# Optimization experiments

Hardware: AMD Instinct MI355X
Metric: run time of the kernel (lower is better)

## Reference

```python
import jax, jax.numpy as jnp
import numpy as np

SCALAR_DIM = 452          # 2 + 6 + (110+1)*4
GRID_C, GRID_H, GRID_W = 2, 32, 18
GRID_FLAT = GRID_C * GRID_H * GRID_W  # 1152
OBS_DIM = SCALAR_DIM + GRID_FLAT      # 1604
CNN_OUT, SC_OUT, HID, N_ACT = 128, 64, 128, 2305
CNN_FLAT = 64 * 8 * 5                 # 32x18 -> 16x9 -> 8x5
T, B = 256, 128


def setup_inputs() -> dict:
    key = jax.random.key(0)
    ks = jax.random.split(key, 24)
    p = lambda k, shape: jax.random.normal(k, shape, jnp.float32) * 0.02
    return dict(
        obs_seq=jax.random.uniform(ks[0], (T, B, OBS_DIM), jnp.float32),
        h0=jnp.zeros((1, B, HID), jnp.float32),
        c0=jnp.zeros((1, B, HID), jnp.float32),
        done_mask=jax.random.randint(ks[1], (T, B), 0, 2) > 0,
        conv1_w=p(ks[2], (32, GRID_C, 3, 3)), conv1_b=jnp.zeros((32,), jnp.float32),
        conv2_w=p(ks[3], (64, 32, 3, 3)),     conv2_b=jnp.zeros((64,), jnp.float32),
        conv3_w=p(ks[4], (64, 64, 3, 3)),     conv3_b=jnp.zeros((64,), jnp.float32),
        fc_w=p(ks[5], (CNN_OUT, CNN_FLAT)),   fc_b=jnp.zeros((CNN_OUT,), jnp.float32),
        s1_w=p(ks[6], (64, SCALAR_DIM)),      s1_b=jnp.zeros((64,), jnp.float32),
        s2_w=p(ks[7], (SC_OUT, 64)),          s2_b=jnp.zeros((SC_OUT,), jnp.float32),
        w_ih=p(ks[8], (4 * HID, CNN_OUT + SC_OUT)),
        w_hh=p(ks[9], (4 * HID, HID)),
        b_ih=jnp.zeros((4 * HID,), jnp.float32),
        b_hh=jnp.zeros((4 * HID,), jnp.float32),
        pol_w=p(ks[10], (N_ACT, HID)), pol_b=jnp.zeros((N_ACT,), jnp.float32),
        val_w=p(ks[11], (1, HID)),     val_b=jnp.zeros((1,), jnp.float32),
    )


def _conv(x, w, b, stride):
    y = jax.lax.conv_general_dilated(
        x, w, (stride, stride), ((1, 1), (1, 1)),
        dimension_numbers=("NCHW", "OIHW", "NCHW"))
    return y + b[None, :, None, None]


def reference(obs_seq, h0, c0, done_mask,
              conv1_w, conv1_b, conv2_w, conv2_b, conv3_w, conv3_b,
              fc_w, fc_b, s1_w, s1_b, s2_w, s2_b,
              w_ih, w_hh, b_ih, b_hh, pol_w, pol_b, val_w, val_b):
    Tt, Bb, _ = obs_seq.shape
    flat = obs_seq.reshape(Tt * Bb, -1)
    scalars = flat[:, :SCALAR_DIM]
    grid = flat[:, SCALAR_DIM:SCALAR_DIM + GRID_FLAT].reshape(-1, GRID_C, GRID_H, GRID_W)

    # CNN encoder
    x = jax.nn.relu(_conv(grid, conv1_w, conv1_b, 1))
    x = jax.nn.relu(_conv(x, conv2_w, conv2_b, 2))
    x = jax.nn.relu(_conv(x, conv3_w, conv3_b, 2))
    cnn = jax.nn.relu(x.reshape(x.shape[0], -1) @ fc_w.T + fc_b)

    # scalar MLP
    sc = jax.nn.relu(jax.nn.relu(scalars @ s1_w.T + s1_b) @ s2_w.T + s2_b)

    emb = jnp.concatenate([cnn, sc], axis=-1).reshape(Tt, Bb, -1)  # (T,B,192)

    # episode-reset mask applied BEFORE each step (for t>0, from done[t-1])
    keep = jnp.concatenate(
        [jnp.ones((1, Bb), jnp.float32),
         1.0 - done_mask[:-1].astype(jnp.float32)], axis=0)[..., None]  # (T,B,1)

    def step(carry, inp):
        h, c = carry
        x_t, k_t = inp
        h = h * k_t
        c = c * k_t
        g = x_t @ w_ih.T + h @ w_hh.T + b_ih + b_hh
        i, f, gg, o = jnp.split(g, 4, axis=-1)  # torch gate order i,f,g,o
        c = jax.nn.sigmoid(f) * c + jax.nn.sigmoid(i) * jnp.tanh(gg)
        h = jax.nn.sigmoid(o) * jnp.tanh(c)
        return (h, c), h

    (h_f, c_f), outs = jax.lax.scan(step, (h0[0], c0[0]), (emb, keep))

    logits = outs @ pol_w.T + pol_b   # (T,B,n_actions)
    values = outs @ val_w.T + val_b   # (T,B,1)
    return logits, values, h_f[None], c_f[None]
```

## Files before the change

kernel.cpp:

```cpp
#include <hip/hip_runtime.h>


typedef __attribute__((ext_vector_type(8))) short v8s;
typedef __attribute__((ext_vector_type(4))) float v4f;
typedef __attribute__((ext_vector_type(4))) unsigned int v4u;

#define DEV static __device__ __forceinline__

DEV unsigned int cvtpk(float lo, float hi){
  unsigned int d;
  asm("v_cvt_pk_bf16_f32 %0, %1, %2" : "=v"(d) : "v"(lo), "v"(hi));
  return d;
}
DEV unsigned short f2bf(float x){ return (unsigned short)(cvtpk(x, x) & 0xffffu); }
DEV float bf2f(unsigned short h){ return __uint_as_float(((unsigned int)h) << 16); }
DEV unsigned int pkbf(float a, float b){ return cvtpk(a, b); }
DEV v4f MFMA(v8s a, v8s b, v4f c){ return __builtin_amdgcn_mfma_f32_16x16x32_bf16(a, b, c, 0, 0, 0); }
DEV v4f vzero(){ v4f z = {0.f, 0.f, 0.f, 0.f}; return z; }
DEV float relu(float x){ return x > 0.f ? x : 0.f; }
DEV float sigm(float x){ return 1.0f / (1.0f + __expf(-x)); }
DEV float tanhfast(float x){
  x = fminf(15.0f, fmaxf(-15.0f, x));
  float e = __expf(2.0f * x);
  return (e - 1.0f) / (e + 1.0f);
}
DEV uint2 pack4(v4f a, float4 b){
  return make_uint2(cvtpk(relu(a[0]+b.x), relu(a[1]+b.y)),
                    cvtpk(relu(a[2]+b.z), relu(a[3]+b.w)));
}
union U8S { v4u u4; v8s s8; };

__global__ __launch_bounds__(256) void pack_kernel(
    const float* __restrict__ src, const float* __restrict__ src2,
    unsigned short* __restrict__ dst, int N, int K, int KS, int CI, int mode, int total){
  for (int idx = blockIdx.x * 256 + threadIdx.x; idx < total; idx += gridDim.x * 256){
    int e  = idx & 7;
    int l  = (idx >> 3) & 63;
    int fs = idx >> 9;
    int ks = fs % KS;
    int nt = fs / KS;
    int n = nt * 16 + (l & 15);
    int k = ks * 32 + (l >> 4) * 8 + e;
    float v = 0.f;
    if (n < N && k < K){
      if (mode == 0)      v = src[n * K + k];
      else if (mode == 1){ int p9 = k / CI, ci = k - p9 * CI; v = src[(n * CI + ci) * 9 + p9]; }
      else if (mode == 2){ int pos = k >> 6, ci = k & 63;     v = src[n * 2560 + ci * 40 + pos]; }
      else if (mode == 3) v = (k < 192) ? src[n * 192 + k] : src2[n * 128 + (k - 192)];
      else { int dy = k >> 3, r = k & 7, dx = r >> 1, ci = r & 1;
             if (dx < 3) v = src[(n * 2 + ci) * 9 + dy * 3 + dx]; }
    }
    dst[idx] = f2bf(v);
  }
}

__global__ __launch_bounds__(512) void bias_kernel(const float* __restrict__ bih,
    const float* __restrict__ bhh, float* __restrict__ bias512){
  int t = threadIdx.x;
  if (t < 512) bias512[t] = bih[t] + bhh[t];
}

__global__ __launch_bounds__(256) void mlp_kernel(const float* __restrict__ obs,
    const unsigned short* __restrict__ s1p, const unsigned short* __restrict__ s2p,
    const float* __restrict__ s1b, const float* __restrict__ s2b,
    unsigned short* __restrict__ emb){
  __shared__ __align__(16) unsigned short xl[32 * 488];
  __shared__ __align__(16) unsigned short h1[32 * 72];
  int tid = threadIdx.x, w = tid >> 6, l = tid & 63, i = l & 15, u = l >> 4;
  long s0 = (long)blockIdx.x * 32;
  for (int idx = tid; idx < 32 * 113; idx += 256){
    int r = idx / 113, q = idx - r * 113;
    float4 v = *(const float4*)&obs[(s0 + r) * 1604 + q * 4];
    *(uint2*)&xl[r * 488 + q * 4] = make_uint2(pkbf(v.x, v.y), pkbf(v.z, v.w));
  }
  for (int idx = tid; idx < 32 * 28; idx += 256){
    int r = idx / 28, k = 452 + (idx - r * 28);
    xl[r * 488 + k] = 0;
  }
  __syncthreads();
  v4f acc0 = vzero(), acc1 = vzero();
  const v8s* F1 = (const v8s*)s1p;
  #pragma unroll
  for (int ks = 0; ks < 15; ++ks){
    v8s bb = F1[(w * 15 + ks) * 64 + l];
    v8s aa0 = *(const v8s*)&xl[(0 * 16 + i) * 488 + ks * 32 + u * 8];
    v8s aa1 = *(const v8s*)&xl[(1 * 16 + i) * 488 + ks * 32 + u * 8];
    acc0 = MFMA(aa0, bb, acc0);
    acc1 = MFMA(aa1, bb, acc1);
  }
  float b1 = s1b[w * 16 + i];
  #pragma unroll
  for (int r = 0; r < 4; ++r){
    float v0 = relu(acc0[r] + b1);
    float v1 = relu(acc1[r] + b1);
    h1[(u * 4 + r) * 72 + w * 16 + i] = f2bf(v0);
    h1[(16 + u * 4 + r) * 72 + w * 16 + i] = f2bf(v1);
  }
  __syncthreads();
  v4f a20 = vzero(), a21 = vzero();
  const v8s* F2 = (const v8s*)s2p;
  #pragma unroll
  for (int ks = 0; ks < 2; ++ks){
    v8s bb = F2[(w * 2 + ks) * 64 + l];
    v8s aa0 = *(const v8s*)&h1[(0 * 16 + i) * 72 + ks * 32 + u * 8];
    v8s aa1 = *(const v8s*)&h1[(1 * 16 + i) * 72 + ks * 32 + u * 8];
    a20 = MFMA(aa0, bb, a20);
    a21 = MFMA(aa1, bb, a21);
  }
  float b2 = s2b[w * 16 + i];
  #pragma unroll
  for (int r = 0; r < 4; ++r){
    float v0 = relu(a20[r] + b2);
    float v1 = relu(a21[r] + b2);
    emb[(s0 + u * 4 + r) * 192 + 128 + w * 16 + i] = f2bf(v0);
    emb[(s0 + 16 + u * 4 + r) * 192 + 128 + w * 16 + i] = f2bf(v1);
  }
}

#define ACT1o 0
#define ACT2o 43520
#define GRIDo 68864
#define SWZ(p) ((((p) >> 1) & 7) << 4)

__global__ __launch_bounds__(256, 2) void conv_kernel(const float* __restrict__ obs,
    const unsigned short* __restrict__ w1p, const unsigned short* __restrict__ w2p,
    const unsigned short* __restrict__ w3p,
    const float* __restrict__ b1v, const float* __restrict__ b2v, const float* __restrict__ b3v,
    unsigned short* __restrict__ act3g){
  __shared__ __align__(16) char lds[74496];
  int tid = threadIdx.x, w = tid >> 6, l = tid & 63, i = l & 15, u = l >> 4;
  int nh = w & 1, mh = w >> 1;
  const v8s* W1 = (const v8s*)w1p;
  const v8s* W2 = (const v8s*)w2p;
  const v8s* W3 = (const v8s*)w3p;
  v8s w1f0 = W1[l], w1f1 = W1[64 + l];
  float4 bc1a = *(const float4*)&b1v[u * 4];
  float4 bc1b = *(const float4*)&b1v[16 + u * 4];
  float4 bc2a = *(const float4*)&b2v[nh * 32 + u * 4];
  float4 bc2b = *(const float4*)&b2v[nh * 32 + 16 + u * 4];
  float4 bc3a = *(const float4*)&b3v[nh * 32 + u * 4];
  float4 bc3b = *(const float4*)&b3v[nh * 32 + 16 + u * 4];
  for (int idx = tid; idx < 18624; idx += 256) *(unsigned int*)(lds + idx * 4) = 0u;
  int soff[4];
  #pragma unroll
  for (int j = 0; j < 4; ++j){
    int p = tid * 4 + j, r = p / 18, c = p - r * 18;
    soff[j] = ((r + 1) * 20 + (c + 1)) * 4;
  }
  __syncthreads();
  long sbase = (long)blockIdx.x * 64;
  if (tid < 144){
    const float4* gp = (const float4*)(obs + sbase * 1604 + 452);
    float4 a = gp[tid], b = gp[tid + 144];
    *(unsigned int*)(lds + GRIDo + soff[0]) = pkbf(a.x, b.x);
    *(unsigned int*)(lds + GRIDo + soff[1]) = pkbf(a.y, b.y);
    *(unsigned int*)(lds + GRIDo + soff[2]) = pkbf(a.z, b.z);
    *(unsigned int*)(lds + GRIDo + soff[3]) = pkbf(a.w, b.w);
  }
  __syncthreads();

  int pos3_0 = (mh ? 1 : 0) * 16 + i;
  int pos3_1r = 32 + i;
  int pos3_1 = pos3_1r > 39 ? 39 : pos3_1r;
  int oh30 = pos3_0 / 5, ow30 = pos3_0 - oh30 * 5;
  int oh31 = pos3_1 / 5, ow31 = pos3_1 - oh31 * 5;
  int pr3_0 = (2 * oh30) * 11 + 2 * ow30;
  int pr3_1 = (2 * oh31) * 11 + 2 * ow31;

  for (int it = 0; it < 64; ++it){
    long s = sbase + it;
    int gbo = GRIDo + (it & 1) * 2816;
    int z2; asm("s_mov_b32 %0, 0" : "=s"(z2) : "s"(it));
    v8s w2f[2][9];
    #pragma unroll
    for (int jj = 0; jj < 2; ++jj)
      #pragma unroll
      for (int t = 0; t < 9; ++t) w2f[jj][t] = W2[((nh * 2 + jj) * 9 + t) * 64 + l + z2];
    float4 pa, pb; bool pf = (it < 63) && (tid < 144);
    if (pf){
      const float4* gp = (const float4*)(obs + (s + 1) * 1604 + 452);
      pa = gp[tid]; pb = gp[tid + 144];
    }
    #pragma unroll
    for (int k = 0; k < 9; ++k){
      int ntl = w + 4 * k;
      int pos = ntl * 16 + i;
      int oh = pos / 18, ow = pos - oh * 18;
      int glin = gbo + ((oh + u) * 20 + ow) * 4;
      U8S gv;
      gv.u4.x = *(const unsigned int*)(lds + glin);
      gv.u4.y = *(const unsigned int*)(lds + glin + 4);
      gv.u4.z = *(const unsigned int*)(lds + glin + 8);
      gv.u4.w = *(const unsigned int*)(lds + glin + 12);
      v4f a0 = MFMA(w1f0, gv.s8, vzero());
      v4f a1 = MFMA(w1f1, gv.s8, vzero());
      int p1 = (oh + 1) * 20 + (ow + 1);
      int sA = SWZ(p1);
      *(uint2*)(lds + ACT1o + ((p1 * 64 + u * 8) ^ sA))      = pack4(a0, bc1a);
      *(uint2*)(lds + ACT1o + ((p1 * 64 + 32 + u * 8) ^ sA)) = pack4(a1, bc1b);
    }
    __syncthreads();
    #pragma unroll
    for (int kk = 0; kk < 5; ++kk){
      int ntl = mh + 2 * kk;
      if (ntl < 9){
        int pos2 = ntl * 16 + i;
        int oh = pos2 / 9, ow = pos2 - oh * 9;
        int pr0 = (2 * oh) * 20 + 2 * ow;
        v4f a0 = vzero(), a1 = vzero();
        #pragma unroll
        for (int dy = 0; dy < 3; ++dy)
          #pragma unroll
          for (int dx = 0; dx < 3; ++dx){
            int p = pr0 + dy * 20 + dx;
            int byte = (p * 64 + u * 16) ^ SWZ(p);
            v8s bf = *(const v8s*)(lds + ACT1o + byte);
            a0 = MFMA(w2f[0][dy * 3 + dx], bf, a0);
            a1 = MFMA(w2f[1][dy * 3 + dx], bf, a1);
          }
        int p2 = (oh + 1) * 11 + (ow + 1);
        int sB = SWZ(p2);
        *(uint2*)(lds + ACT2o + ((p2 * 128 + nh * 64 + u * 8) ^ sB))      = pack4(a0, bc2a);
        *(uint2*)(lds + ACT2o + ((p2 * 128 + nh * 64 + 32 + u * 8) ^ sB)) = pack4(a1, bc2b);
      }
    }
    if (pf){
      int gbn = GRIDo + ((it + 1) & 1) * 2816;
      *(unsigned int*)(lds + gbn + soff[0]) = pkbf(pa.x, pb.x);
      *(unsigned int*)(lds + gbn + soff[1]) = pkbf(pa.y, pb.y);
      *(unsigned int*)(lds + gbn + soff[2]) = pkbf(pa.z, pb.z);
      *(unsigned int*)(lds + gbn + soff[3]) = pkbf(pa.w, pb.w);
    }
    __syncthreads();
    int z3; asm("s_mov_b32 %0, 0" : "=s"(z3) : "s"(it));
    v4f c300 = vzero(), c301 = vzero(), c310 = vzero(), c311 = vzero();
    #pragma unroll
    for (int ksh = 0; ksh < 2; ++ksh){
      const int t0 = ksh * 5, tc = ksh ? 4 : 5;
      v8s w3q[2][5][2];
      #pragma unroll
      for (int j = 0; j < 2; ++j)
        #pragma unroll
        for (int tt = 0; tt < 5; ++tt){
          if (tt < tc){
            #pragma unroll
            for (int h = 0; h < 2; ++h)
              w3q[j][tt][h] = W3[((2 * nh + j) * 18 + 2 * (t0 + tt) + h) * 64 + l + z3];
          }
        }
      #pragma unroll
      for (int tt = 0; tt < 5; ++tt){
        if (tt < tc){
          int tap = t0 + tt, dy = tap / 3, dx = tap - dy * 3;
          int dpp = dy * 11 + dx;
          #pragma unroll
          for (int h = 0; h < 2; ++h){
            {
              int p = pr3_0 + dpp;
              int byte = (p * 128 + h * 64 + u * 16) ^ SWZ(p);
              v8s bf = *(const v8s*)(lds + ACT2o + byte);
              c300 = MFMA(w3q[0][tt][h], bf, c300);
              c301 = MFMA(w3q[1][tt][h], bf, c301);
            }
            if (mh == 0){
              int p = pr3_1 + dpp;
              int byte = (p * 128 + h * 64 + u * 16) ^ SWZ(p);
              v8s bf = *(const v8s*)(lds + ACT2o + byte);
              c310 = MFMA(w3q[0][tt][h], bf, c310);
              c311 = MFMA(w3q[1][tt][h], bf, c311);
            }
          }
        }
      }
    }
    {
      unsigned short* dg = act3g + s * 2560;
      *(uint2*)(dg + pos3_0 * 64 + nh * 32 + u * 4)      = pack4(c300, bc3a);
      *(uint2*)(dg + pos3_0 * 64 + nh * 32 + 16 + u * 4) = pack4(c301, bc3b);
      if (mh == 0 && pos3_1r < 40){
        *(uint2*)(dg + pos3_1r * 64 + nh * 32 + u * 4)      = pack4(c310, bc3a);
        *(uint2*)(dg + pos3_1r * 64 + nh * 32 + 16 + u * 4) = pack4(c311, bc3b);
      }
    }
  }
}

__global__ __launch_bounds__(256) void fc_kernel(const unsigned short* __restrict__ act3g,
    const unsigned short* __restrict__ fcp, const float* __restrict__ fcb,
    unsigned short* __restrict__ emb){
  __shared__ __align__(16) unsigned short al[64 * 264];
  int tid = threadIdx.x, w = tid >> 6, l = tid & 63, i = l & 15, u = l >> 4;
  long s0 = (long)blockIdx.x * 64;
  v4f acc[4][2];
  #pragma unroll
  for (int mt = 0; mt < 4; ++mt){ acc[mt][0] = vzero(); acc[mt][1] = vzero(); }
  const v8s* F = (const v8s*)fcp;
  for (int kc = 0; kc < 10; ++kc){
    __syncthreads();
    for (int idx = tid; idx < 64 * 32; idx += 256){
      int r = idx >> 5, q = idx & 31;
      *(v8s*)&al[r * 264 + q * 8] = *(const v8s*)&act3g[(s0 + r) * 2560 + kc * 256 + q * 8];
    }
    __syncthreads();
    #pragma unroll
    for (int ksl = 0; ksl < 8; ++ksl){
      v8s b0 = F[((w * 2 + 0) * 80 + kc * 8 + ksl) * 64 + l];
      v8s b1 = F[((w * 2 + 1) * 80 + kc * 8 + ksl) * 64 + l];
      #pragma unroll
      for (int mt = 0; mt < 4; ++mt){
        v8s aa = *(const v8s*)&al[(mt * 16 + i) * 264 + ksl * 32 + u * 8];
        acc[mt][0] = MFMA(aa, b0, acc[mt][0]);
        acc[mt][1] = MFMA(aa, b1, acc[mt][1]);
      }
    }
  }
  float fb0 = fcb[(w * 2) * 16 + i], fb1 = fcb[(w * 2 + 1) * 16 + i];
  #pragma unroll
  for (int mt = 0; mt < 4; ++mt)
    #pragma unroll
    for (int r = 0; r < 4; ++r){
      float v0 = relu(acc[mt][0][r] + fb0);
      float v1 = relu(acc[mt][1][r] + fb1);
      emb[(s0 + mt * 16 + u * 4 + r) * 192 + (w * 2) * 16 + i] = f2bf(v0);
      emb[(s0 + mt * 16 + u * 4 + r) * 192 + (w * 2 + 1) * 16 + i] = f2bf(v1);
    }
}

__global__ __launch_bounds__(256) void segprep_kernel(const void* __restrict__ dmask,
    unsigned int* __restrict__ segs, int4* __restrict__ gtab, int* __restrict__ meta){
  __shared__ int cnt[257], off[257], place[257];
  __shared__ int notInt;
  int tid = threadIdx.x;
  for (int idx = tid; idx < 257; idx += 256){ cnt[idx] = 0; place[idx] = 0; }
  if (tid == 0) notInt = 0;
  __syncthreads();
  const unsigned char* p8 = (const unsigned char*)dmask;
  int nz = 0;
  for (int idx = tid; idx < 2048; idx += 256)
    if (p8[idx * 4 + 1] | p8[idx * 4 + 2] | p8[idx * 4 + 3]) nz = 1;
  if (nz) notInt = 1;
  __syncthreads();
  bool m32 = (notInt == 0);
  const int* p32 = (const int*)dmask;
  if (tid < 128){
    int b = tid, ts = 0;
    for (int t = 0; t < 256; ++t){
      bool d = (t == 255) ? true : (m32 ? (p32[t * 128 + b] != 0) : (p8[t * 128 + b] != 0));
      if (d){ atomicAdd(&cnt[t - ts + 1], 1); ts = t + 1; }
    }
  }
  __syncthreads();
  if (tid == 0){
    int acc = 0;
    for (int len = 1; len <= 256; ++len){ off[len] = acc; acc += cnt[len]; }
    int G = 0;
    for (int len = 1; len <= 256; ++len){
      int c = cnt[len], g = 0;
      while (c > 0){
        int take = c < 32 ? c : 32;
        gtab[G] = make_int4(len, off[len] + g * 32, take, 0);
        ++G; c -= 32; ++g;
      }
    }
    meta[0] = G;
  }
  __syncthreads();
  if (tid < 128){
    int b = tid, ts = 0;
    for (int t = 0; t < 256; ++t){
      bool d = (t == 255) ? true : (m32 ? (p32[t * 128 + b] != 0) : (p8[t * 128 + b] != 0));
      if (d){
        int len = t - ts + 1;
        int slot = off[len] + atomicAdd(&place[len], 1);
        segs[slot] = (unsigned int)(b | (ts << 8));
        ts = t + 1;
      }
    }
  }
}

__global__ __launch_bounds__(512) void lstm_kernel(
    const unsigned short* __restrict__ emb, const unsigned short* __restrict__ lstmp,
    const float* __restrict__ bias512,
    const float* __restrict__ h0, const float* __restrict__ c0,
    const unsigned int* __restrict__ segs, const int4* __restrict__ gtab,
    const int* __restrict__ meta,
    unsigned short* __restrict__ outsb, float* __restrict__ hf, float* __restrict__ cf){
  int grp = blockIdx.x;
  if (grp >= meta[0]) return;
  int4 gd = gtab[grp];
  int len = gd.x, base = gd.y, nseg = gd.z;
  __shared__ __align__(16) unsigned short hbuf[2][32 * 136];
  __shared__ int sb[32], st[32];
  int tid = threadIdx.x, w = tid >> 6, l = tid & 63, i = l & 15, u = l >> 4;
  if (tid < 32){
    unsigned int sv = segs[base + (tid < nseg ? tid : 0)];
    sb[tid] = (int)(sv & 127u);
    st[tid] = (int)((sv >> 8) & 255u);
  }
  __syncthreads();
  int j = w * 16 + i;
  float cst[2][4];
  #pragma unroll
  for (int mt = 0; mt < 2; ++mt)
    #pragma unroll
    for (int r = 0; r < 4; ++r){
      int slot = mt * 16 + u * 4 + r;
      float cv = 0.f, hv = 0.f;
      if (st[slot] == 0){ cv = c0[sb[slot] * 128 + j]; hv = h0[sb[slot] * 128 + j]; }
      cst[mt][r] = cv;
      hbuf[0][slot * 136 + j] = f2bf(hv);
    }
  float bi = bias512[j], bff = bias512[128 + j], bg = bias512[256 + j], bo = bias512[384 + j];
  int bA0 = sb[i], tA0 = st[i];
  int bA1 = sb[16 + i], tA1 = st[16 + i];
  __syncthreads();
  const v8s* LP = (const v8s*)lstmp;
  for (int step = 0; step < len; ++step){
    int pb = step & 1;
    v4f gi0 = vzero(), gi1 = vzero(), gf0 = vzero(), gf1 = vzero();
    v4f gg0 = vzero(), gg1 = vzero(), go0 = vzero(), go1 = vzero();
    #pragma unroll
    for (int ks = 0; ks < 10; ++ks){
      v8s a0, a1;
      if (ks < 6){
        a0 = *(const v8s*)&emb[((long)(tA0 + step) * 128 + bA0) * 192 + ks * 32 + u * 8];
        a1 = *(const v8s*)&emb[((long)(tA1 + step) * 128 + bA1) * 192 + ks * 32 + u * 8];
      } else {
        int koff = (ks - 6) * 32 + u * 8;
        a0 = *(const v8s*)&hbuf[pb][i * 136 + koff];
        a1 = *(const v8s*)&hbuf[pb][(16 + i) * 136 + koff];
      }
      v8s b_i = LP[((w) * 10 + ks) * 64 + l];
      v8s b_f = LP[((w + 8) * 10 + ks) * 64 + l];
      v8s b_g = LP[((w + 16) * 10 + ks) * 64 + l];
      v8s b_o = LP[((w + 24) * 10 + ks) * 64 + l];
      gi0 = MFMA(a0, b_i, gi0); gi1 = MFMA(a1, b_i, gi1);
      gf0 = MFMA(a0, b_f, gf0); gf1 = MFMA(a1, b_f, gf1);
      gg0 = MFMA(a0, b_g, gg0); gg1 = MFMA(a1, b_g, gg1);
      go0 = MFMA(a0, b_o, go0); go1 = MFMA(a1, b_o, go1);
    }
    #pragma unroll
    for (int mt = 0; mt < 2; ++mt)
      #pragma unroll
      for (int r = 0; r < 4; ++r){
        int slot = mt * 16 + u * 4 + r;
        float giv = mt ? gi1[r] : gi0[r];
        float gfv = mt ? gf1[r] : gf0[r];
        float ggv = mt ? gg1[r] : gg0[r];
        float gov = mt ? go1[r] : go0[r];
        float iv = sigm(giv + bi);
        float fv = sigm(gfv + bff);
        float gv = tanhfast(ggv + bg);
        float ov = sigm(gov + bo);
        float cv = fv * cst[mt][r] + iv * gv;
        cst[mt][r] = cv;
        float hv = ov * tanhfast(cv);
        unsigned short hb = f2bf(hv);
        hbuf[pb ^ 1][slot * 136 + j] = hb;
        if (slot < nseg){
          outsb[((long)(st[slot] + step) * 128 + sb[slot]) * 128 + j] = hb;
          if (st[slot] + len == 256 && step == len - 1){
            hf[sb[slot] * 128 + j] = hv;
            cf[sb[slot] * 128 + j] = cv;
          }
        }
      }
    __syncthreads();
  }
}

__global__ __launch_bounds__(256) void heads_kernel(const unsigned short* __restrict__ outsb,
    const unsigned short* __restrict__ polp, const float* __restrict__ polb,
    float* __restrict__ logits){
  __shared__ __align__(16) unsigned short al[64 * 136];
  int tid = threadIdx.x, w = tid >> 6, l = tid & 63, i = l & 15, u = l >> 4;
  long s0 = (long)blockIdx.x * 64;
  for (int idx = tid; idx < 64 * 16; idx += 256){
    int r = idx >> 4, q = idx & 15;
    *(v8s*)&al[r * 136 + q * 8] = *(const v8s*)&outsb[(s0 + r) * 128 + q * 8];
  }
  __syncthreads();
  v8s af[4][4];
  #pragma unroll
  for (int mt = 0; mt < 4; ++mt)
    #pragma unroll
    for (int ks = 0; ks < 4; ++ks)
      af[mt][ks] = *(const v8s*)&al[(mt * 16 + i) * 136 + ks * 32 + u * 8];
  const v8s* P = (const v8s*)polp;
  for (int nt = w; nt < 145; nt += 4){
    v4f acc[4];
    #pragma unroll
    for (int mt = 0; mt < 4; ++mt) acc[mt] = vzero();
    #pragma unroll
    for (int ks = 0; ks < 4; ++ks){
      v8s bb = P[(nt * 4 + ks) * 64 + l];
      #pragma unroll
      for (int mt = 0; mt < 4; ++mt) acc[mt] = MFMA(af[mt][ks], bb, acc[mt]);
    }
    int n = nt * 16 + i;
    if (n < 2305){
      float pbv = polb[n];
      #pragma unroll
      for (int mt = 0; mt < 4; ++mt)
        #pragma unroll
        for (int r = 0; r < 4; ++r)
          logits[(s0 + mt * 16 + u * 4 + r) * 2305 + n] = acc[mt][r] + pbv;
    }
  }
}

__global__ __launch_bounds__(256) void values_kernel(const unsigned short* __restrict__ outsb,
    const float* __restrict__ vw, const float* __restrict__ vb, float* __restrict__ values){
  int tid = threadIdx.x, w = tid >> 6, l = tid & 63;
  int i16 = l & 15, g = l >> 4;
  float vwf[8];
  #pragma unroll
  for (int e = 0; e < 8; ++e) vwf[e] = vw[i16 * 8 + e];
  float vb0 = vb[0];
  for (int itr = 0; itr < 8; ++itr){
    int row = blockIdx.x * 128 + w * 32 + itr * 4 + g;
    const unsigned short* rp = outsb + (size_t)row * 128 + i16 * 8;
    v8s xv = *(const v8s*)rp;
    float acc = 0.f;
    #pragma unroll
    for (int e = 0; e < 8; ++e) acc += bf2f((unsigned short)xv[e]) * vwf[e];
    acc += __shfl_xor(acc, 1, 16);
    acc += __shfl_xor(acc, 2, 16);
    acc += __shfl_xor(acc, 4, 16);
    acc += __shfl_xor(acc, 8, 16);
    if (i16 == 0) values[row] = acc + vb0;
  }
}

extern "C" void kernel_launch(void* const* d_in, const int* in_sizes, int n_in,
                              void* d_out, int out_size, void* d_ws, size_t ws_size,
                              hipStream_t stream){
  (void)in_sizes; (void)n_in; (void)out_size; (void)ws_size;
  const float* obs = (const float*)d_in[0];
  const float* h0  = (const float*)d_in[1];
  const float* c0  = (const float*)d_in[2];
  const void*  dm  = d_in[3];
  const float* c1w = (const float*)d_in[4];  const float* c1b = (const float*)d_in[5];
  const float* c2w = (const float*)d_in[6];  const float* c2b = (const float*)d_in[7];
  const float* c3w = (const float*)d_in[8];  const float* c3b = (const float*)d_in[9];
  const float* fcw = (const float*)d_in[10]; const float* fcb = (const float*)d_in[11];
  const float* s1w = (const float*)d_in[12]; const float* s1b = (const float*)d_in[13];
  const float* s2w = (const float*)d_in[14]; const float* s2b = (const float*)d_in[15];
  const float* wih = (const float*)d_in[16]; const float* whh = (const float*)d_in[17];
  const float* bih = (const float*)d_in[18]; const float* bhh = (const float*)d_in[19];
  const float* pw  = (const float*)d_in[20]; const float* pb  = (const float*)d_in[21];
  const float* vw  = (const float*)d_in[22]; const float* vb  = (const float*)d_in[23];

  char* ws = (char*)d_ws;
  size_t off = 0;
  auto take = [&](size_t sz)->char*{
    char* p = ws + off; off = (off + sz + 255) & ~(size_t)255; return p;
  };
  unsigned short* emb    = (unsigned short*)take(32768UL * 192 * 2);
  unsigned short* outsb  = (unsigned short*)take(32768UL * 128 * 2);
  unsigned short* w1p    = (unsigned short*)take(1024UL * 2);
  unsigned short* w2p    = (unsigned short*)take(18432UL * 2);
  unsigned short* w3p    = (unsigned short*)take(36864UL * 2);
  unsigned short* fcp    = (unsigned short*)take(327680UL * 2);
  unsigned short* s1p    = (unsigned short*)take(30720UL * 2);
  unsigned short* s2p    = (unsigned short*)take(4096UL * 2);
  unsigned short* lsp    = (unsigned short*)take(163840UL * 2);
  unsigned short* pop    = (unsigned short*)take(296960UL * 2);
  float*          b512   = (float*)take(512UL * 4);
  unsigned int*   segs   = (unsigned int*)take(32768UL * 4);
  int4*           gtab   = (int4*)take(1280UL * 16);
  int*            meta   = (int*)take(256);

  float* outp   = (float*)d_out;
  float* logits = outp;
  float* values = outp + 75530240L;
  float* hf     = outp + 75563008L;
  float* cf     = outp + 75579392L;
  unsigned short* act3g = (unsigned short*)d_out;

  dim3 b256(256), b512t(512);
  pack_kernel<<<dim3(4),    b256, 0, stream>>>(c1w, nullptr, w1p, 32, 24, 1, 2, 4, 1024);
  pack_kernel<<<dim3(72),   b256, 0, stream>>>(c2w, nullptr, w2p, 64, 288, 9, 32, 1, 18432);
  pack_kernel<<<dim3(144),  b256, 0, stream>>>(c3w, nullptr, w3p, 64, 576, 18, 64, 1, 36864);
  pack_kernel<<<dim3(1280), b256, 0, stream>>>(fcw, nullptr, fcp, 128, 2560, 80, 0, 2, 327680);
  pack_kernel<<<dim3(120),  b256, 0, stream>>>(s1w, nullptr, s1p, 64, 452, 15, 0, 0, 30720);
  pack_kernel<<<dim3(16),   b256, 0, stream>>>(s2w, nullptr, s2p, 64, 64, 2, 0, 0, 4096);
  pack_kernel<<<dim3(640),  b256, 0, stream>>>(wih, whh,     lsp, 512, 320, 10, 0, 3, 163840);
  pack_kernel<<<dim3(1160), b256, 0, stream>>>(pw,  nullptr, pop, 2305, 128, 4, 0, 0, 296960);
  bias_kernel<<<dim3(1), b512t, 0, stream>>>(bih, bhh, b512);
  segprep_kernel<<<dim3(1), b256, 0, stream>>>(dm, segs, gtab, meta);
  mlp_kernel<<<dim3(1024), b256, 0, stream>>>(obs, s1p, s2p, s1b, s2b, emb);
  conv_kernel<<<dim3(512), b256, 0, stream>>>(obs, w1p, w2p, w3p, c1b, c2b, c3b, act3g);
  fc_kernel<<<dim3(512), b256, 0, stream>>>(act3g, fcp, fcb, emb);
  lstm_kernel<<<dim3(1280), b512t, 0, stream>>>(emb, lsp, b512, h0, c0, segs, gtab, meta,
                                                outsb, hf, cf);
  heads_kernel<<<dim3(512), b256, 0, stream>>>(outsb, pop, pb, logits);
  values_kernel<<<dim3(256), b256, 0, stream>>>(outsb, vw, vb, values);
}
```

Before: 1.117 ms.

## Merge pack launches, widen conv kernel to 512 threads, fold values into heads

Replaces eight weight-pack launches with one kernel that picks its job by block index, cutting launch overhead. The conv kernel moves from 256 to 512 threads per block, spreading the conv1, conv2 and conv3 tiles over eight waves. Six waves now compute conv3, which removes the uneven second tile that waves with mh==0 handled before. The value head is computed inside the heads kernel from the activations already in LDS, removing a separate launch and a re-read of the LSTM outputs. The larger blocks raise register pressure per block under the new launch bounds and leave some waves idle during conv3.

```diff
diff --git a/kernel.cpp b/kernel.cpp
--- a/kernel.cpp
+++ b/kernel.cpp
@@ -30,28 +30,45 @@
 }
 union U8S { v4u u4; v8s s8; };
 
-__global__ __launch_bounds__(256) void pack_kernel(
-    const float* __restrict__ src, const float* __restrict__ src2,
-    unsigned short* __restrict__ dst, int N, int K, int KS, int CI, int mode, int total){
-  for (int idx = blockIdx.x * 256 + threadIdx.x; idx < total; idx += gridDim.x * 256){
-    int e  = idx & 7;
-    int l  = (idx >> 3) & 63;
-    int fs = idx >> 9;
-    int ks = fs % KS;
-    int nt = fs / KS;
-    int n = nt * 16 + (l & 15);
-    int k = ks * 32 + (l >> 4) * 8 + e;
-    float v = 0.f;
-    if (n < N && k < K){
-      if (mode == 0)      v = src[n * K + k];
-      else if (mode == 1){ int p9 = k / CI, ci = k - p9 * CI; v = src[(n * CI + ci) * 9 + p9]; }
-      else if (mode == 2){ int pos = k >> 6, ci = k & 63;     v = src[n * 2560 + ci * 40 + pos]; }
-      else if (mode == 3) v = (k < 192) ? src[n * 192 + k] : src2[n * 128 + (k - 192)];
-      else { int dy = k >> 3, r = k & 7, dx = r >> 1, ci = r & 1;
-             if (dx < 3) v = src[(n * 2 + ci) * 9 + dy * 3 + dx]; }
-    }
-    dst[idx] = f2bf(v);
-  }
+__global__ __launch_bounds__(256) void pack_all(
+    const float* __restrict__ c1w, const float* __restrict__ c2w,
+    const float* __restrict__ c3w, const float* __restrict__ fcw,
+    const float* __restrict__ s1w, const float* __restrict__ s2w,
+    const float* __restrict__ wih, const float* __restrict__ whh,
+    const float* __restrict__ pw,
+    unsigned short* __restrict__ w1p, unsigned short* __restrict__ w2p,
+    unsigned short* __restrict__ w3p, unsigned short* __restrict__ fcp,
+    unsigned short* __restrict__ s1p, unsigned short* __restrict__ s2p,
+    unsigned short* __restrict__ lsp, unsigned short* __restrict__ pop){
+  int b = blockIdx.x;
+  const float *src, *src2 = nullptr; unsigned short* dst;
+  int N, K, KS, CI, mode, rel;
+  if      (b < 4)   { src=c1w; dst=w1p; N=32;  K=24;  KS=1;  CI=2;  mode=4; rel=b; }
+  else if (b < 76)  { src=c2w; dst=w2p; N=64;  K=288; KS=9;  CI=32; mode=1; rel=b-4; }
+  else if (b < 220) { src=c3w; dst=w3p; N=64;  K=576; KS=18; CI=64; mode=1; rel=b-76; }
+  else if (b < 1500){ src=fcw; dst=fcp; N=128; K=2560;KS=80; CI=0;  mode=2; rel=b-220; }
+  else if (b < 1620){ src=s1w; dst=s1p; N=64;  K=452; KS=15; CI=0;  mode=0; rel=b-1500; }
+  else if (b < 1636){ src=s2w; dst=s2p; N=64;  K=64;  KS=2;  CI=0;  mode=0; rel=b-1620; }
+  else if (b < 2276){ src=wih; src2=whh; dst=lsp; N=512; K=320; KS=10; CI=0; mode=3; rel=b-1636; }
+  else              { src=pw;  dst=pop; N=2305;K=128; KS=4;  CI=0;  mode=0; rel=b-2276; }
+  int idx = rel * 256 + threadIdx.x;
+  int e  = idx & 7;
+  int l  = (idx >> 3) & 63;
+  int fs = idx >> 9;
+  int ks = fs % KS;
+  int nt = fs / KS;
+  int n = nt * 16 + (l & 15);
+  int k = ks * 32 + (l >> 4) * 8 + e;
+  float v = 0.f;
+  if (n < N && k < K){
+    if (mode == 0)      v = src[n * K + k];
+    else if (mode == 1){ int p9 = k / CI, ci = k - p9 * CI; v = src[(n * CI + ci) * 9 + p9]; }
+    else if (mode == 2){ int pos = k >> 6, ci = k & 63;     v = src[n * 2560 + ci * 40 + pos]; }
+    else if (mode == 3) v = (k < 192) ? src[n * 192 + k] : src2[n * 128 + (k - 192)];
+    else { int dy = k >> 3, r = k & 7, dx = r >> 1, ci = r & 1;
+           if (dx < 3) v = src[(n * 2 + ci) * 9 + dy * 3 + dx]; }
+  }
+  dst[idx] = f2bf(v);
 }
 
 __global__ __launch_bounds__(512) void bias_kernel(const float* __restrict__ bih,
@@ -122,25 +139,26 @@
 #define GRIDo 68864
 #define SWZ(p) ((((p) >> 1) & 7) << 4)
 
-__global__ __launch_bounds__(256, 2) void conv_kernel(const float* __restrict__ obs,
+__global__ __launch_bounds__(512, 4) void conv_kernel(const float* __restrict__ obs,
     const unsigned short* __restrict__ w1p, const unsigned short* __restrict__ w2p,
     const unsigned short* __restrict__ w3p,
     const float* __restrict__ b1v, const float* __restrict__ b2v, const float* __restrict__ b3v,
     unsigned short* __restrict__ act3g){
   __shared__ __align__(16) char lds[74496];
   int tid = threadIdx.x, w = tid >> 6, l = tid & 63, i = l & 15, u = l >> 4;
-  int nh = w & 1, mh = w >> 1;
+  int nh2 = w & 1, pt2 = w >> 1;
+  int cp = w & 1, t3 = w >> 1;
   const v8s* W1 = (const v8s*)w1p;
   const v8s* W2 = (const v8s*)w2p;
   const v8s* W3 = (const v8s*)w3p;
   v8s w1f0 = W1[l], w1f1 = W1[64 + l];
   float4 bc1a = *(const float4*)&b1v[u * 4];
   float4 bc1b = *(const float4*)&b1v[16 + u * 4];
-  float4 bc2a = *(const float4*)&b2v[nh * 32 + u * 4];
-  float4 bc2b = *(const float4*)&b2v[nh * 32 + 16 + u * 4];
-  float4 bc3a = *(const float4*)&b3v[nh * 32 + u * 4];
-  float4 bc3b = *(const float4*)&b3v[nh * 32 + 16 + u * 4];
-  for (int idx = tid; idx < 18624; idx += 256) *(unsigned int*)(lds + idx * 4) = 0u;
+  float4 bc2a = *(const float4*)&b2v[nh2 * 32 + u * 4];
+  float4 bc2b = *(const float4*)&b2v[nh2 * 32 + 16 + u * 4];
+  float4 bc3a = *(const float4*)&b3v[cp * 32 + u * 4];
+  float4 bc3b = *(const float4*)&b3v[cp * 32 + 16 + u * 4];
+  for (int idx = tid; idx < 18624; idx += 512) *(unsigned int*)(lds + idx * 4) = 0u;
   int soff[4];
   #pragma unroll
   for (int j = 0; j < 4; ++j){
@@ -159,13 +177,10 @@
   }
   __syncthreads();
 
-  int pos3_0 = (mh ? 1 : 0) * 16 + i;
-  int pos3_1r = 32 + i;
-  int pos3_1 = pos3_1r > 39 ? 39 : pos3_1r;
-  int oh30 = pos3_0 / 5, ow30 = pos3_0 - oh30 * 5;
-  int oh31 = pos3_1 / 5, ow31 = pos3_1 - oh31 * 5;
-  int pr3_0 = (2 * oh30) * 11 + 2 * ow30;
-  int pr3_1 = (2 * oh31) * 11 + 2 * ow31;
+  int praw3 = t3 * 16 + i;
+  int pos3 = praw3 > 39 ? 39 : praw3;
+  int oh3 = pos3 / 5, ow3 = pos3 - oh3 * 5;
+  int pr3 = (2 * oh3) * 11 + 2 * ow3;
 
   for (int it = 0; it < 64; ++it){
     long s = sbase + it;
@@ -175,34 +190,36 @@
     #pragma unroll
     for (int jj = 0; jj < 2; ++jj)
       #pragma unroll
-      for (int t = 0; t < 9; ++t) w2f[jj][t] = W2[((nh * 2 + jj) * 9 + t) * 64 + l + z2];
+      for (int t = 0; t < 9; ++t) w2f[jj][t] = W2[((nh2 * 2 + jj) * 9 + t) * 64 + l + z2];
     float4 pa, pb; bool pf = (it < 63) && (tid < 144);
     if (pf){
       const float4* gp = (const float4*)(obs + (s + 1) * 1604 + 452);
       pa = gp[tid]; pb = gp[tid + 144];
     }
     #pragma unroll
-    for (int k = 0; k < 9; ++k){
-      int ntl = w + 4 * k;
-      int pos = ntl * 16 + i;
-      int oh = pos / 18, ow = pos - oh * 18;
-      int glin = gbo + ((oh + u) * 20 + ow) * 4;
-      U8S gv;
-      gv.u4.x = *(const unsigned int*)(lds + glin);
-      gv.u4.y = *(const unsigned int*)(lds + glin + 4);
-      gv.u4.z = *(const unsigned int*)(lds + glin + 8);
-      gv.u4.w = *(const unsigned int*)(lds + glin + 12);
-      v4f a0 = MFMA(w1f0, gv.s8, vzero());
-      v4f a1 = MFMA(w1f1, gv.s8, vzero());
-      int p1 = (oh + 1) * 20 + (ow + 1);
-      int sA = SWZ(p1);
-      *(uint2*)(lds + ACT1o + ((p1 * 64 + u * 8) ^ sA))      = pack4(a0, bc1a);
-      *(uint2*)(lds + ACT1o + ((p1 * 64 + 32 + u * 8) ^ sA)) = pack4(a1, bc1b);
+    for (int k = 0; k < 5; ++k){
+      int ntl = w + 8 * k;
+      if (ntl < 36){
+        int pos = ntl * 16 + i;
+        int oh = pos / 18, ow = pos - oh * 18;
+        int glin = gbo + ((oh + u) * 20 + ow) * 4;
+        U8S gv;
+        gv.u4.x = *(const unsigned int*)(lds + glin);
+        gv.u4.y = *(const unsigned int*)(lds + glin + 4);
+        gv.u4.z = *(const unsigned int*)(lds + glin + 8);
+        gv.u4.w = *(const unsigned int*)(lds + glin + 12);
+        v4f a0 = MFMA(w1f0, gv.s8, vzero());
+        v4f a1 = MFMA(w1f1, gv.s8, vzero());
+        int p1 = (oh + 1) * 20 + (ow + 1);
+        int sA = SWZ(p1);
+        *(uint2*)(lds + ACT1o + ((p1 * 64 + u * 8) ^ sA))      = pack4(a0, bc1a);
+        *(uint2*)(lds + ACT1o + ((p1 * 64 + 32 + u * 8) ^ sA)) = pack4(a1, bc1b);
+      }
     }
     __syncthreads();
     #pragma unroll
-    for (int kk = 0; kk < 5; ++kk){
-      int ntl = mh + 2 * kk;
+    for (int kk = 0; kk < 3; ++kk){
+      int ntl = pt2 + 4 * kk;
       if (ntl < 9){
         int pos2 = ntl * 16 + i;
         int oh = pos2 / 9, ow = pos2 - oh * 9;
@@ -220,8 +237,8 @@
           }
         int p2 = (oh + 1) * 11 + (ow + 1);
         int sB = SWZ(p2);
-        *(uint2*)(lds + ACT2o + ((p2 * 128 + nh * 64 + u * 8) ^ sB))      = pack4(a0, bc2a);
-        *(uint2*)(lds + ACT2o + ((p2 * 128 + nh * 64 + 32 + u * 8) ^ sB)) = pack4(a1, bc2b);
+        *(uint2*)(lds + ACT2o + ((p2 * 128 + nh2 * 64 + u * 8) ^ sB))      = pack4(a0, bc2a);
+        *(uint2*)(lds + ACT2o + ((p2 * 128 + nh2 * 64 + 32 + u * 8) ^ sB)) = pack4(a1, bc2b);
       }
     }
     if (pf){
@@ -232,54 +249,43 @@
       *(unsigned int*)(lds + gbn + soff[3]) = pkbf(pa.w, pb.w);
     }
     __syncthreads();
-    int z3; asm("s_mov_b32 %0, 0" : "=s"(z3) : "s"(it));
-    v4f c300 = vzero(), c301 = vzero(), c310 = vzero(), c311 = vzero();
-    #pragma unroll
-    for (int ksh = 0; ksh < 2; ++ksh){
-      const int t0 = ksh * 5, tc = ksh ? 4 : 5;
-      v8s w3q[2][5][2];
+    if (w < 6){
+      int z3; asm("s_mov_b32 %0, 0" : "=s"(z3) : "s"(it));
+      v4f c30 = vzero(), c31 = vzero();
       #pragma unroll
-      for (int j = 0; j < 2; ++j)
+      for (int ksh = 0; ksh < 2; ++ksh){
+        const int t0 = ksh * 5, tc = ksh ? 4 : 5;
+        v8s w3q[2][5][2];
+        #pragma unroll
+        for (int j = 0; j < 2; ++j)
+          #pragma unroll
+          for (int tt = 0; tt < 5; ++tt){
+            if (tt < tc){
+              #pragma unroll
+              for (int h = 0; h < 2; ++h)
+                w3q[j][tt][h] = W3[((2 * cp + j) * 18 + 2 * (t0 + tt) + h) * 64 + l + z3];
+            }
+          }
         #pragma unroll
         for (int tt = 0; tt < 5; ++tt){
           if (tt < tc){
+            int tap = t0 + tt, dy = tap / 3, dx = tap - dy * 3;
+            int dpp = dy * 11 + dx;
             #pragma unroll
-            for (int h = 0; h < 2; ++h)
-              w3q[j][tt][h] = W3[((2 * nh + j) * 18 + 2 * (t0 + tt) + h) * 64 + l + z3];
-          }
-        }
-      #pragma unroll
-      for (int tt = 0; tt < 5; ++tt){
-        if (tt < tc){
-          int tap = t0 + tt, dy = tap / 3, dx = tap - dy * 3;
-          int dpp = dy * 11 + dx;
-          #pragma unroll
-          for (int h = 0; h < 2; ++h){
-            {
-              int p = pr3_0 + dpp;
+            for (int h = 0; h < 2; ++h){
+              int p = pr3 + dpp;
               int byte = (p * 128 + h * 64 + u * 16) ^ SWZ(p);
               v8s bf = *(const v8s*)(lds + ACT2o + byte);
-              c300 = MFMA(w3q[0][tt][h], bf, c300);
-              c301 = MFMA(w3q[1][tt][h], bf, c301);
-            }
-            if (mh == 0){
-              int p = pr3_1 + dpp;
-              int byte = (p * 128 + h * 64 + u * 16) ^ SWZ(p);
-              v8s bf = *(const v8s*)(lds + ACT2o + byte);
-              c310 = MFMA(w3q[0][tt][h], bf, c310);
-              c311 = MFMA(w3q[1][tt][h], bf, c311);
+              c30 = MFMA(w3q[0][tt][h], bf, c30);
+              c31 = MFMA(w3q[1][tt][h], bf, c31);
             }
           }
         }
       }
-    }
-    {
-      unsigned short* dg = act3g + s * 2560;
-      *(uint2*)(dg + pos3_0 * 64 + nh * 32 + u * 4)      = pack4(c300, bc3a);
-      *(uint2*)(dg + pos3_0 * 64 + nh * 32 + 16 + u * 4) = pack4(c301, bc3b);
-      if (mh == 0 && pos3_1r < 40){
-        *(uint2*)(dg + pos3_1r * 64 + nh * 32 + u * 4)      = pack4(c310, bc3a);
-        *(uint2*)(dg + pos3_1r * 64 + nh * 32 + 16 + u * 4) = pack4(c311, bc3b);
+      if (praw3 < 40){
+        unsigned short* dg = act3g + s * 2560;
+        *(uint2*)(dg + praw3 * 64 + cp * 32 + u * 4)      = pack4(c30, bc3a);
+        *(uint2*)(dg + praw3 * 64 + cp * 32 + 16 + u * 4) = pack4(c31, bc3b);
       }
     }
   }
@@ -472,7 +478,8 @@
 
 __global__ __launch_bounds__(256) void heads_kernel(const unsigned short* __restrict__ outsb,
     const unsigned short* __restrict__ polp, const float* __restrict__ polb,
-    float* __restrict__ logits){
+    const float* __restrict__ vw, const float* __restrict__ vb,
+    float* __restrict__ logits, float* __restrict__ values){
   __shared__ __align__(16) unsigned short al[64 * 136];
   int tid = threadIdx.x, w = tid >> 6, l = tid & 63, i = l & 15, u = l >> 4;
   long s0 = (long)blockIdx.x * 64;
@@ -508,29 +515,20 @@
           logits[(s0 + mt * 16 + u * 4 + r) * 2305 + n] = acc[mt][r] + pbv;
     }
   }
-}
-
-__global__ __launch_bounds__(256) void values_kernel(const unsigned short* __restrict__ outsb,
-    const float* __restrict__ vw, const float* __restrict__ vb, float* __restrict__ values){
-  int tid = threadIdx.x, w = tid >> 6, l = tid & 63;
-  int i16 = l & 15, g = l >> 4;
-  float vwf[8];
-  #pragma unroll
-  for (int e = 0; e < 8; ++e) vwf[e] = vw[i16 * 8 + e];
-  float vb0 = vb[0];
-  for (int itr = 0; itr < 8; ++itr){
-    int row = blockIdx.x * 128 + w * 32 + itr * 4 + g;
-    const unsigned short* rp = outsb + (size_t)row * 128 + i16 * 8;
-    v8s xv = *(const v8s*)rp;
-    float acc = 0.f;
-    #pragma unroll
-    for (int e = 0; e < 8; ++e) acc += bf2f((unsigned short)xv[e]) * vwf[e];
-    acc += __shfl_xor(acc, 1, 16);
-    acc += __shfl_xor(acc, 2, 16);
-    acc += __shfl_xor(acc, 4, 16);
-    acc += __shfl_xor(acc, 8, 16);
-    if (i16 == 0) values[row] = acc + vb0;
-  }
+  float vacc = 0.f;
+  #pragma unroll
+  for (int g = 0; g < 4; ++g){
+    float4 vA = *(const float4*)&vw[g * 32 + u * 8];
+    float4 vB = *(const float4*)&vw[g * 32 + u * 8 + 4];
+    v8s xv = *(const v8s*)&al[(w * 16 + i) * 136 + g * 32 + u * 8];
+    vacc += bf2f((unsigned short)xv[0]) * vA.x + bf2f((unsigned short)xv[1]) * vA.y
+          + bf2f((unsigned short)xv[2]) * vA.z + bf2f((unsigned short)xv[3]) * vA.w
+          + bf2f((unsigned short)xv[4]) * vB.x + bf2f((unsigned short)xv[5]) * vB.y
+          + bf2f((unsigned short)xv[6]) * vB.z + bf2f((unsigned short)xv[7]) * vB.w;
+  }
+  vacc += __shfl_xor(vacc, 16);
+  vacc += __shfl_xor(vacc, 32);
+  if (u == 0) values[s0 + w * 16 + i] = vacc + vb[0];
 }
 
 extern "C" void kernel_launch(void* const* d_in, const int* in_sizes, int n_in,
@@ -580,21 +578,14 @@
   unsigned short* act3g = (unsigned short*)d_out;
 
   dim3 b256(256), b512t(512);
-  pack_kernel<<<dim3(4),    b256, 0, stream>>>(c1w, nullptr, w1p, 32, 24, 1, 2, 4, 1024);
-  pack_kernel<<<dim3(72),   b256, 0, stream>>>(c2w, nullptr, w2p, 64, 288, 9, 32, 1, 18432);
-  pack_kernel<<<dim3(144),  b256, 0, stream>>>(c3w, nullptr, w3p, 64, 576, 18, 64, 1, 36864);
-  pack_kernel<<<dim3(1280), b256, 0, stream>>>(fcw, nullptr, fcp, 128, 2560, 80, 0, 2, 327680);
-  pack_kernel<<<dim3(120),  b256, 0, stream>>>(s1w, nullptr, s1p, 64, 452, 15, 0, 0, 30720);
-  pack_kernel<<<dim3(16),   b256, 0, stream>>>(s2w, nullptr, s2p, 64, 64, 2, 0, 0, 4096);
-  pack_kernel<<<dim3(640),  b256, 0, stream>>>(wih, whh,     lsp, 512, 320, 10, 0, 3, 163840);
-  pack_kernel<<<dim3(1160), b256, 0, stream>>>(pw,  nullptr, pop, 2305, 128, 4, 0, 0, 296960);
+  pack_all<<<dim3(3436), b256, 0, stream>>>(c1w, c2w, c3w, fcw, s1w, s2w, wih, whh, pw,
+                                            w1p, w2p, w3p, fcp, s1p, s2p, lsp, pop);
   bias_kernel<<<dim3(1), b512t, 0, stream>>>(bih, bhh, b512);
   segprep_kernel<<<dim3(1), b256, 0, stream>>>(dm, segs, gtab, meta);
   mlp_kernel<<<dim3(1024), b256, 0, stream>>>(obs, s1p, s2p, s1b, s2b, emb);
-  conv_kernel<<<dim3(512), b256, 0, stream>>>(obs, w1p, w2p, w3p, c1b, c2b, c3b, act3g);
+  conv_kernel<<<dim3(512), b512t, 0, stream>>>(obs, w1p, w2p, w3p, c1b, c2b, c3b, act3g);
   fc_kernel<<<dim3(512), b256, 0, stream>>>(act3g, fcp, fcb, emb);
   lstm_kernel<<<dim3(1280), b512t, 0, stream>>>(emb, lsp, b512, h0, c0, segs, gtab, meta,
                                                 outsb, hf, cf);
-  heads_kernel<<<dim3(512), b256, 0, stream>>>(outsb, pop, pb, logits);
-  values_kernel<<<dim3(256), b256, 0, stream>>>(outsb, vw, vb, values);
-}
+  heads_kernel<<<dim3(512), b256, 0, stream>>>(outsb, pop, pb, vw, vb, logits, values);
+}
```

After: 1.873 ms. 67.8% more time.
